# Kernel tuning notes

Hardware: AMD Instinct MI355X
Metric: run time of the kernel (lower is better)

## Reference

```python
import jax, jax.numpy as jnp
import numpy as np

G, NPG, C, H, F, L = 256, 128, 16, 128, 128, 3
N = G * NPG          # 32768 nodes
E = 524288           # 16 edges per node on average
REG, REG_C = 0.01, 0.01
LN_EPS = 1e-5


def setup_inputs() -> dict:
    key = jax.random.key(0)
    ks = jax.random.split(key, 20)
    x = jax.random.normal(ks[0], (N, F), dtype=jnp.float32)
    # edges kept within each graph so dense pooling matches to_dense_batch semantics
    epg = E // G
    offs = jnp.repeat(jnp.arange(G, dtype=jnp.int64) * NPG, epg)
    src = jax.random.randint(ks[1], (E,), 0, NPG, dtype=jnp.int64) + offs
    tgt = jax.random.randint(ks[2], (E,), 0, NPG, dtype=jnp.int64) + offs
    edge_index = jnp.stack([src, tgt])
    mask_breaks = jax.random.bernoulli(ks[3], 0.5, (E,))
    s = jax.random.uniform(ks[4], (N, C), dtype=jnp.float32)
    batch = jnp.repeat(jnp.arange(G, dtype=jnp.int64), NPG)
    sc = 1.0 / np.sqrt(H)
    Wn = jax.random.normal(ks[5], (L, H, H), dtype=jnp.float32) * sc
    bn_ = jax.random.normal(ks[6], (L, H), dtype=jnp.float32) * sc
    Wo = jax.random.normal(ks[7], (L, H, H), dtype=jnp.float32) * sc
    bo = jax.random.normal(ks[8], (L, H), dtype=jnp.float32) * sc
    Wr = jax.random.normal(ks[9], (L, H, H), dtype=jnp.float32) * sc
    ln_g = jnp.ones((L, H), dtype=jnp.float32)
    ln_b = jnp.zeros((L, H), dtype=jnp.float32)
    fln_g = jnp.ones((H,), dtype=jnp.float32)
    fln_b = jnp.zeros((H,), dtype=jnp.float32)
    lin_w = jax.random.normal(ks[10], (1, H), dtype=jnp.float32) * sc
    bias = jnp.zeros((1,), dtype=jnp.float32)
    return {"x": x, "edge_index": edge_index, "mask_breaks": mask_breaks, "s": s,
            "batch": batch, "Wn": Wn, "bn_": bn_, "Wo": Wo, "bo": bo, "Wr": Wr,
            "ln_g": ln_g, "ln_b": ln_b, "fln_g": fln_g, "fln_b": fln_b,
            "lin_w": lin_w, "bias": bias}


def _layernorm(h, g, b):
    mu = jnp.mean(h, axis=-1, keepdims=True)
    v = jnp.mean(jnp.square(h - mu), axis=-1, keepdims=True)
    return (h - mu) * jax.lax.rsqrt(v + LN_EPS) * g + b


def reference(x, edge_index, mask_breaks, s, batch, Wn, bn_, Wo, bo, Wr,
              ln_g, ln_b, fln_g, fln_b, lin_w, bias):
    src, tgt = edge_index[0], edge_index[1]
    ones_e = jnp.ones((E,), dtype=x.dtype)
    cnt = jax.ops.segment_sum(ones_e, tgt, num_segments=N)          # in-degree
    inv_cnt = (1.0 / jnp.maximum(cnt, 1.0))[:, None]
    h = x
    for i in range(L):
        x_in = h @ Wn[i].T + bn_[i]
        x_out = h @ Wo[i].T + bo[i]
        x_root = h @ Wr[i].T
        msg = jnp.where(mask_breaks[:, None], x_in[src], x_out[src])  # [E,H]
        agg = jax.ops.segment_sum(msg, tgt, num_segments=N) * inv_cnt  # mean aggr
        h = jax.nn.relu(_layernorm(agg + x_root, ln_g[i], ln_b[i]))
    # dense per-graph views (equal-size graphs, batch ids sorted -> reshape)
    xd = h.reshape(G, NPG, H)
    sd = s.reshape(G, NPG, C)
    pooled = jnp.einsum("gnc,gnh->gch", sd, xd)                      # [G,C,H]
    pooled = _layernorm(pooled, fln_g, fln_b)
    xc = pooled @ lin_w.T                                            # [G,C,1]
    col_sum = sd.sum(axis=1)                                          # [G,C]
    cmask = (col_sum > 0)[..., None]
    xc = xc * cmask.astype(xc.dtype)
    out = xc.sum(axis=1) + bias                                      # [G,1]
    reg_loss = jnp.abs(Wo).sum() + jnp.abs(bo).sum()
    denom = (cmask.astype(xc.dtype).squeeze(-1) + 1e-7).sum(axis=1, keepdims=True)
    l1_loss = (jnp.abs(xc).sum(axis=1) / denom).mean()
    losses = REG * reg_loss + REG_C * l1_loss
    return out, losses, xc
```

## Files before the change

kernel.cpp:

```cpp
#include <hip/hip_runtime.h>

#define NN   32768
#define HD   128
#define EE   524288
#define GG   256
#define EPG  2048
#define CCd  16
#define LLd  3

typedef short short8 __attribute__((ext_vector_type(8)));
typedef float f32x4 __attribute__((ext_vector_type(4)));

__device__ __forceinline__ unsigned short f2bf(float f) {
  unsigned u = __builtin_bit_cast(unsigned, f);
  return (unsigned short)((u + 0x7FFFu + ((u >> 16) & 1u)) >> 16);
}
__device__ __forceinline__ unsigned bfpack(float a, float b) {
  return (unsigned)f2bf(a) | ((unsigned)f2bf(b) << 16);
}

__global__ __launch_bounds__(256) void convert_w_kernel(const float* __restrict__ Wn, const float* __restrict__ Wo,
                                                        const float* __restrict__ Wr, const float* __restrict__ bo,
                                                        unsigned* __restrict__ Wnb, unsigned* __restrict__ Wob,
                                                        unsigned* __restrict__ Wrb, float* __restrict__ wsreg) {
  int i = blockIdx.x * 256 + threadIdx.x;
  float4 a = *(const float4*)(Wn + (size_t)i * 4);
  float4 b = *(const float4*)(Wo + (size_t)i * 4);
  float4 c = *(const float4*)(Wr + (size_t)i * 4);
  *(uint2*)(Wnb + (size_t)i * 2) = make_uint2(bfpack(a.x, a.y), bfpack(a.z, a.w));
  *(uint2*)(Wob + (size_t)i * 2) = make_uint2(bfpack(b.x, b.y), bfpack(b.z, b.w));
  *(uint2*)(Wrb + (size_t)i * 2) = make_uint2(bfpack(c.x, c.y), bfpack(c.z, c.w));
  float s = fabsf(b.x) + fabsf(b.y) + fabsf(b.z) + fabsf(b.w);
  if (blockIdx.x == 0 && threadIdx.x < 96) {
    float4 d = *(const float4*)(bo + threadIdx.x * 4);
    s += fabsf(d.x) + fabsf(d.y) + fabsf(d.z) + fabsf(d.w);
  }
#pragma unroll
  for (int mk = 1; mk < 64; mk <<= 1) s += __shfl_xor(s, mk, 64);
  if ((threadIdx.x & 63) == 0) atomicAdd(wsreg, s);
}

__global__ __launch_bounds__(256) void build_m_kernel(const int* __restrict__ src, const int* __restrict__ tgt,
                                                      const int* __restrict__ mask,
                                                      unsigned* __restrict__ Mb, float* __restrict__ fin,
                                                      float* __restrict__ fout) {
  __shared__ unsigned Mi[2 * 128 * 64];
  const int g = blockIdx.x;
  const int tid = threadIdx.x;
  for (int i = tid; i < 16384; i += 256) Mi[i] = 0;
  __syncthreads();
  const int e0 = g * EPG;
#pragma unroll
  for (int i = 0; i < 8; ++i) {
    int e = e0 + i * 256 + tid;
    int t = tgt[e] & 127;
    int sl = src[e] & 127;
    int dir = (mask[e] != 0) ? 0 : 1;
    atomicAdd(&Mi[dir * 8192 + t * 64 + (sl >> 1)], 1u << ((sl & 1) * 16));
  }
  __syncthreads();
  const int t = tid >> 1, p = tid & 1;
  unsigned nin = 0, nout = 0;
#pragma unroll 4
  for (int k = 0; k < 32; ++k) { unsigned v = Mi[t * 64 + p * 32 + k]; nin += (v & 0xffffu) + (v >> 16); }
#pragma unroll 4
  for (int k = 0; k < 32; ++k) { unsigned v = Mi[8192 + t * 64 + p * 32 + k]; nout += (v & 0xffffu) + (v >> 16); }
  nin += __shfl_xor((int)nin, 1);
  nout += __shfl_xor((int)nout, 1);
  unsigned dg = nin + nout;
  float inv = 1.0f / (float)(dg > 0 ? dg : 1);
  if (p == 0) { fin[g * 128 + t] = (float)nin * inv; fout[g * 128 + t] = (float)nout * inv; }
#pragma unroll
  for (int dir = 0; dir < 2; ++dir) {
    int base = dir * 8192 + t * 64 + p * 32;
#pragma unroll
    for (int k4 = 0; k4 < 8; ++k4) {
      uint4 v = *(const uint4*)&Mi[base + k4 * 4];
      uint4 o;
      o.x = bfpack((float)(v.x & 0xffffu) * inv, (float)(v.x >> 16) * inv);
      o.y = bfpack((float)(v.y & 0xffffu) * inv, (float)(v.y >> 16) * inv);
      o.z = bfpack((float)(v.z & 0xffffu) * inv, (float)(v.z >> 16) * inv);
      o.w = bfpack((float)(v.w & 0xffffu) * inv, (float)(v.w >> 16) * inv);
      *(uint4*)&Mb[(size_t)g * 16384 + base + k4 * 4] = o;
    }
  }
}

#define SSTR 136
#define YSTR 40
__global__ __launch_bounds__(512) void fused_kernel(
    const float* __restrict__ x, const unsigned short* __restrict__ Mb,
    const unsigned short* __restrict__ Wnb, const unsigned short* __restrict__ Wob,
    const unsigned short* __restrict__ Wrb,
    const float* __restrict__ bn, const float* __restrict__ bo,
    const float* __restrict__ fin, const float* __restrict__ fout,
    const float* __restrict__ lng, const float* __restrict__ lnb,
    const float* __restrict__ s,
    const float* __restrict__ flng, const float* __restrict__ flnb,
    const float* __restrict__ linw, const float* __restrict__ bias,
    float* __restrict__ out, float* __restrict__ l1g) {
  __shared__ unsigned short scratch[128 * SSTR];
  __shared__ unsigned short ys[2 * 128 * YSTR];
  __shared__ unsigned short sTs[16 * SSTR];
  __shared__ float colsumS[CCd];
  __shared__ float xcs[CCd], axcs[CCd], msk[CCd];

  const int g = blockIdx.x;
  const int tid = threadIdx.x;
  const int wave = tid >> 6;
  const int lane = tid & 63;
  const int m = lane & 15;
  const int q = lane >> 4;
  const unsigned short* Mg = Mb + (size_t)g * 32768;
  unsigned* scratch32 = (unsigned*)scratch;

  {
    const float4* xg = (const float4*)(x + (size_t)g * 16384);
#pragma unroll
    for (int i = 0; i < 8; ++i) {
      int flat = i * 512 + tid;
      int t = flat >> 5, f = (flat & 31) << 2;
      float4 v = xg[flat];
      int w0 = (t * SSTR + f) >> 1;
      scratch32[w0] = bfpack(v.x, v.y);
      scratch32[w0 + 1] = bfpack(v.z, v.w);
    }
    int t = tid >> 2, c0 = (tid & 3) << 2;
    float4 v = *(const float4*)(s + (size_t)g * 2048 + t * 16 + c0);
    sTs[(c0 + 0) * SSTR + t] = f2bf(v.x);
    sTs[(c0 + 1) * SSTR + t] = f2bf(v.y);
    sTs[(c0 + 2) * SSTR + t] = f2bf(v.z);
    sTs[(c0 + 3) * SSTR + t] = f2bf(v.w);
    if (tid < CCd) {
      float cs = 0.f;
      for (int tt = 0; tt < 128; ++tt) cs += s[(size_t)g * 2048 + tt * 16 + tid];
      colsumS[tid] = cs;
    }
  }
  __syncthreads();

  for (int L = 0; L < LLd; ++L) {
    const unsigned short* WnL = Wnb + (size_t)L * 16384;
    const unsigned short* WoL = Wob + (size_t)L * 16384;
    const unsigned short* WrL = Wrb + (size_t)L * 16384;
    f32x4 pre[8];
#pragma unroll
    for (int ct = 0; ct < 8; ++ct) pre[ct] = (f32x4){0.f, 0.f, 0.f, 0.f};

#pragma unroll
    for (int ks = 0; ks < 4; ++ks) {
      short8 a = *(const short8*)&scratch[(wave * 16 + m) * SSTR + ks * 32 + q * 8];
#pragma unroll
      for (int ct = 0; ct < 8; ++ct) {
        short8 b = *(const short8*)(WrL + (size_t)(ct * 16 + m) * 128 + ks * 32 + q * 8);
        pre[ct] = __builtin_amdgcn_mfma_f32_16x16x32_bf16(a, b, pre[ct], 0, 0, 0);
      }
    }

    short8 wnf[4], wof[4];
#pragma unroll
    for (int ks = 0; ks < 4; ++ks) {
      wnf[ks] = *(const short8*)(WnL + (size_t)(wave * 16 + m) * 128 + ks * 32 + q * 8);
      wof[ks] = *(const short8*)(WoL + (size_t)(wave * 16 + m) * 128 + ks * 32 + q * 8);
    }

    for (int sc = 0; sc < 4; ++sc) {
      f32x4 ya[2][2];
#pragma unroll
      for (int o2 = 0; o2 < 2; ++o2)
#pragma unroll
        for (int st = 0; st < 2; ++st) ya[o2][st] = (f32x4){0.f, 0.f, 0.f, 0.f};
#pragma unroll
      for (int ks = 0; ks < 4; ++ks) {
        short8 a0 = *(const short8*)&scratch[(sc * 32 + m) * SSTR + ks * 32 + q * 8];
        short8 a1 = *(const short8*)&scratch[(sc * 32 + 16 + m) * SSTR + ks * 32 + q * 8];
        ya[0][0] = __builtin_amdgcn_mfma_f32_16x16x32_bf16(a0, wnf[ks], ya[0][0], 0, 0, 0);
        ya[0][1] = __builtin_amdgcn_mfma_f32_16x16x32_bf16(a1, wnf[ks], ya[0][1], 0, 0, 0);
        ya[1][0] = __builtin_amdgcn_mfma_f32_16x16x32_bf16(a0, wof[ks], ya[1][0], 0, 0, 0);
        ya[1][1] = __builtin_amdgcn_mfma_f32_16x16x32_bf16(a1, wof[ks], ya[1][1], 0, 0, 0);
      }
#pragma unroll
      for (int o2 = 0; o2 < 2; ++o2)
#pragma unroll
        for (int st = 0; st < 2; ++st)
#pragma unroll
          for (int r = 0; r < 4; ++r)
            ys[o2 * 128 * YSTR + (wave * 16 + m) * YSTR + st * 16 + q * 4 + r] = f2bf(ya[o2][st][r]);
      __syncthreads();
#pragma unroll
      for (int o2 = 0; o2 < 2; ++o2) {
        short8 am = *(const short8*)(Mg + (size_t)o2 * 16384 + (size_t)(wave * 16 + m) * 128 + sc * 32 + q * 8);
#pragma unroll
        for (int ct = 0; ct < 8; ++ct) {
          short8 b = *(const short8*)&ys[o2 * 128 * YSTR + (ct * 16 + m) * YSTR + q * 8];
          pre[ct] = __builtin_amdgcn_mfma_f32_16x16x32_bf16(am, b, pre[ct], 0, 0, 0);
        }
      }
      if (sc < 3) __syncthreads();
    }

    float bnv[8], bov[8], gv[8], bv[8];
#pragma unroll
    for (int ct = 0; ct < 8; ++ct) {
      int c = L * 128 + ct * 16 + m;
      bnv[ct] = bn[c]; bov[ct] = bo[c]; gv[ct] = lng[c]; bv[ct] = lnb[c];
    }
#pragma unroll
    for (int r = 0; r < 4; ++r) {
      const int tl = q * 4 + r;
      const int T = g * 128 + wave * 16 + tl;
      const float fiv = fin[T], fov = fout[T];
      float v[8];
      float sum = 0.f;
#pragma unroll
      for (int ct = 0; ct < 8; ++ct) {
        v[ct] = pre[ct][r] + fiv * bnv[ct] + fov * bov[ct];
        sum += v[ct];
      }
      sum += __shfl_xor(sum, 1); sum += __shfl_xor(sum, 2);
      sum += __shfl_xor(sum, 4); sum += __shfl_xor(sum, 8);
      const float mu = sum * (1.0f / 128.0f);
      float sq = 0.f;
#pragma unroll
      for (int ct = 0; ct < 8; ++ct) { float d = v[ct] - mu; sq += d * d; }
      sq += __shfl_xor(sq, 1); sq += __shfl_xor(sq, 2);
      sq += __shfl_xor(sq, 4); sq += __shfl_xor(sq, 8);
      const float rstd = rsqrtf(sq * (1.0f / 128.0f) + 1e-5f);
#pragma unroll
      for (int ct = 0; ct < 8; ++ct) {
        float o = fmaxf((v[ct] - mu) * rstd * gv[ct] + bv[ct], 0.0f);
        scratch[(wave * 16 + tl) * SSTR + ct * 16 + m] = f2bf(o);
      }
    }
    __syncthreads();
  }

  f32x4 pl = (f32x4){0.f, 0.f, 0.f, 0.f};
#pragma unroll
  for (int ks = 0; ks < 4; ++ks) {
    short8 a = *(const short8*)&sTs[m * SSTR + ks * 32 + q * 8];
    short8 b;
#pragma unroll
    for (int j = 0; j < 8; ++j)
      b[j] = (short)scratch[(ks * 32 + q * 8 + j) * SSTR + wave * 16 + m];
    pl = __builtin_amdgcn_mfma_f32_16x16x32_bf16(a, b, pl, 0, 0, 0);
  }
  float* pooledS = (float*)ys;
#pragma unroll
  for (int r = 0; r < 4; ++r) pooledS[(q * 4 + r) * 132 + wave * 16 + m] = pl[r];
  __syncthreads();

  if (tid < 256) {
    const int c = tid >> 4;
    const int j0 = (tid & 15) << 3;
    float v[8];
#pragma unroll
    for (int jj = 0; jj < 8; ++jj) v[jj] = pooledS[c * 132 + j0 + jj];
    float sum = 0.f;
#pragma unroll
    for (int jj = 0; jj < 8; ++jj) sum += v[jj];
#pragma unroll
    for (int mk = 1; mk < 16; mk <<= 1) sum += __shfl_xor(sum, mk, 64);
    float mu = sum * (1.0f / 128.0f);
    float sq = 0.f;
#pragma unroll
    for (int jj = 0; jj < 8; ++jj) { float d = v[jj] - mu; sq += d * d; }
#pragma unroll
    for (int mk = 1; mk < 16; mk <<= 1) sq += __shfl_xor(sq, mk, 64);
    float rstd = rsqrtf(sq * (1.0f / 128.0f) + 1e-5f);
    float dot = 0.f;
#pragma unroll
    for (int jj = 0; jj < 8; ++jj) {
      float nv = (v[jj] - mu) * rstd * flng[j0 + jj] + flnb[j0 + jj];
      dot += nv * linw[j0 + jj];
    }
#pragma unroll
    for (int mk = 1; mk < 16; mk <<= 1) dot += __shfl_xor(dot, mk, 64);
    if ((tid & 15) == 0) {
      float cm = (colsumS[c] > 0.f) ? 1.0f : 0.0f;
      float xcv = dot * cm;
      out[257 + g * CCd + c] = xcv;
      xcs[c] = xcv; axcs[c] = fabsf(xcv); msk[c] = cm;
    }
  }
  __syncthreads();
  if (tid == 0) {
    float so = 0.f, sa = 0.f, sd = 0.f;
#pragma unroll
    for (int k = 0; k < CCd; ++k) { so += xcs[k]; sa += axcs[k]; sd += msk[k] + 1e-7f; }
    out[g] = so + bias[0];
    l1g[g] = sa / sd;
  }
}

__global__ __launch_bounds__(256) void combine_kernel(const float* __restrict__ l1g, const float* __restrict__ wsreg,
                                                      float* __restrict__ outp) {
  const int tid = threadIdx.x;
  float s2 = l1g[tid];
#pragma unroll
  for (int mk = 1; mk < 64; mk <<= 1) s2 += __shfl_xor(s2, mk, 64);
  __shared__ float rs2[4];
  if ((tid & 63) == 0) rs2[tid >> 6] = s2;
  __syncthreads();
  if (tid == 0) {
    float l1 = (rs2[0] + rs2[1] + rs2[2] + rs2[3]) * (1.0f / GG);
    outp[0] = 0.01f * wsreg[0] + 0.01f * l1;
  }
}

extern "C" void kernel_launch(void* const* d_in, const int* in_sizes, int n_in,
                              void* d_out, int out_size, void* d_ws, size_t ws_size,
                              hipStream_t stream) {
  (void)in_sizes; (void)n_in; (void)out_size; (void)ws_size;
  const float* x    = (const float*)d_in[0];
  const int*   ei   = (const int*)d_in[1];
  const int*   mask = (const int*)d_in[2];
  const float* s    = (const float*)d_in[3];
  const float* Wn   = (const float*)d_in[5];
  const float* bn   = (const float*)d_in[6];
  const float* Wo   = (const float*)d_in[7];
  const float* bo   = (const float*)d_in[8];
  const float* Wr   = (const float*)d_in[9];
  const float* lng  = (const float*)d_in[10];
  const float* lnb  = (const float*)d_in[11];
  const float* flng = (const float*)d_in[12];
  const float* flnb = (const float*)d_in[13];
  const float* linw = (const float*)d_in[14];
  const float* bias = (const float*)d_in[15];
  float* out = (float*)d_out;

  char* ws = (char*)d_ws;
  size_t off = 0;
  auto alloc = [&](size_t b) { char* p = ws + off; off += (b + 255) & ~(size_t)255; return p; };
  unsigned short* Mbuf = (unsigned short*)alloc((size_t)GG * 2 * 128 * 128 * 2);
  float* fin    = (float*)alloc((size_t)NN * 4);
  float* fout   = (float*)alloc((size_t)NN * 4);
  unsigned short* Wnb = (unsigned short*)alloc((size_t)LLd * HD * HD * 2);
  unsigned short* Wob = (unsigned short*)alloc((size_t)LLd * HD * HD * 2);
  unsigned short* Wrb = (unsigned short*)alloc((size_t)LLd * HD * HD * 2);
  float* l1g    = (float*)alloc((size_t)GG * 4);
  float* wsreg  = (float*)alloc(256);

  const int* srcA = ei;
  const int* tgtA = ei + EE;

  hipMemsetAsync(wsreg, 0, 4, stream);
  convert_w_kernel<<<LLd * HD * HD / (256 * 4), 256, 0, stream>>>(Wn, Wo, Wr, bo,
      (unsigned*)Wnb, (unsigned*)Wob, (unsigned*)Wrb, wsreg);
  build_m_kernel<<<GG, 256, 0, stream>>>(srcA, tgtA, mask, (unsigned*)Mbuf, fin, fout);
  fused_kernel<<<GG, 512, 0, stream>>>(x, Mbuf, Wnb, Wob, Wrb, bn, bo, fin, fout,
                                       lng, lnb, s, flng, flnb, linw, bias, out, l1g);
  combine_kernel<<<1, 256, 0, stream>>>(l1g, wsreg, out + 256);
}
```

Measured before the change: 163.7 us.

## Merge prep kernels and double-buffer Y tiles in fused GNN layer loop

Merges the weight conversion and adjacency-matrix build into one prep kernel launch, removing a launch. In the fused kernel, the per-chunk Y = h·Wn/Wo products are software-pipelined into a double-buffered LDS tile, so the next chunk's MFMAs overlap the current aggregation and one barrier per step is removed. The adjacency fragments and the fin/fout scalars are hoisted into registers once rather than reloaded every layer. The build-M stores become fully coalesced through a shared inverse-degree table, and the LDS reads are staggered. Costs are more LDS and register pressure, which could lower occupancy.

Measured after the change: 196.2 us. 1.2x slower.

```diff
diff --git a/kernel.cpp b/kernel.cpp
--- a/kernel.cpp
+++ b/kernel.cpp
@@ -7,6 +7,8 @@
 #define EPG  2048
 #define CCd  16
 #define LLd  3
+#define SSTR 136
+#define YSTR 44
 
 typedef short short8 __attribute__((ext_vector_type(8)));
 typedef float f32x4 __attribute__((ext_vector_type(4)));
@@ -18,36 +20,40 @@
 __device__ __forceinline__ unsigned bfpack(float a, float b) {
   return (unsigned)f2bf(a) | ((unsigned)f2bf(b) << 16);
 }
-
-__global__ __launch_bounds__(256) void convert_w_kernel(const float* __restrict__ Wn, const float* __restrict__ Wo,
-                                                        const float* __restrict__ Wr, const float* __restrict__ bo,
-                                                        unsigned* __restrict__ Wnb, unsigned* __restrict__ Wob,
-                                                        unsigned* __restrict__ Wrb, float* __restrict__ wsreg) {
-  int i = blockIdx.x * 256 + threadIdx.x;
-  float4 a = *(const float4*)(Wn + (size_t)i * 4);
-  float4 b = *(const float4*)(Wo + (size_t)i * 4);
-  float4 c = *(const float4*)(Wr + (size_t)i * 4);
-  *(uint2*)(Wnb + (size_t)i * 2) = make_uint2(bfpack(a.x, a.y), bfpack(a.z, a.w));
-  *(uint2*)(Wob + (size_t)i * 2) = make_uint2(bfpack(b.x, b.y), bfpack(b.z, b.w));
-  *(uint2*)(Wrb + (size_t)i * 2) = make_uint2(bfpack(c.x, c.y), bfpack(c.z, c.w));
-  float s = fabsf(b.x) + fabsf(b.y) + fabsf(b.z) + fabsf(b.w);
-  if (blockIdx.x == 0 && threadIdx.x < 96) {
-    float4 d = *(const float4*)(bo + threadIdx.x * 4);
-    s += fabsf(d.x) + fabsf(d.y) + fabsf(d.z) + fabsf(d.w);
-  }
-#pragma unroll
-  for (int mk = 1; mk < 64; mk <<= 1) s += __shfl_xor(s, mk, 64);
-  if ((threadIdx.x & 63) == 0) atomicAdd(wsreg, s);
-}
-
-__global__ __launch_bounds__(256) void build_m_kernel(const int* __restrict__ src, const int* __restrict__ tgt,
-                                                      const int* __restrict__ mask,
-                                                      unsigned* __restrict__ Mb, float* __restrict__ fin,
-                                                      float* __restrict__ fout) {
+#define MFMA __builtin_amdgcn_mfma_f32_16x16x32_bf16
+
+__global__ __launch_bounds__(256) void prep_kernel(const int* __restrict__ src, const int* __restrict__ tgt,
+                                                   const int* __restrict__ mask,
+                                                   const float* __restrict__ Wn, const float* __restrict__ Wo,
+                                                   const float* __restrict__ Wr, const float* __restrict__ bo,
+                                                   unsigned* __restrict__ Mb, float* __restrict__ fin,
+                                                   float* __restrict__ fout,
+                                                   unsigned* __restrict__ Wnb, unsigned* __restrict__ Wob,
+                                                   unsigned* __restrict__ Wrb, float* __restrict__ wsreg) {
   __shared__ unsigned Mi[2 * 128 * 64];
+  __shared__ float invS[128];
+  const int tid = threadIdx.x;
+  if (blockIdx.x >= GG) {
+    int i = (blockIdx.x - GG) * 256 + tid;
+    float4 a = *(const float4*)(Wn + (size_t)i * 4);
+    float4 b = *(const float4*)(Wo + (size_t)i * 4);
+    float4 c = *(const float4*)(Wr + (size_t)i * 4);
+    *(uint2*)(Wnb + (size_t)i * 2) = make_uint2(bfpack(a.x, a.y), bfpack(a.z, a.w));
+    *(uint2*)(Wob + (size_t)i * 2) = make_uint2(bfpack(b.x, b.y), bfpack(b.z, b.w));
+    *(uint2*)(Wrb + (size_t)i * 2) = make_uint2(bfpack(c.x, c.y), bfpack(c.z, c.w));
+    float s = fabsf(b.x) + fabsf(b.y) + fabsf(b.z) + fabsf(b.w);
+    if (blockIdx.x == GG && tid < 96) {
+      float4 d = *(const float4*)(bo + tid * 4);
+      s += fabsf(d.x) + fabsf(d.y) + fabsf(d.z) + fabsf(d.w);
+    }
+#pragma unroll
+    for (int mk = 1; mk < 64; mk <<= 1) s += __shfl_xor(s, mk, 64);
+    if ((tid & 63) == 0) atomicAdd(wsreg, s);
+    return;
+  }
   const int g = blockIdx.x;
-  const int tid = threadIdx.x;
-  for (int i = tid; i < 16384; i += 256) Mi[i] = 0;
+  uint4* Mi4 = (uint4*)Mi;
+  for (int i = tid; i < 4096; i += 256) Mi4[i] = make_uint4(0, 0, 0, 0);
   __syncthreads();
   const int e0 = g * EPG;
 #pragma unroll
@@ -60,34 +66,38 @@
   }
   __syncthreads();
   const int t = tid >> 1, p = tid & 1;
+  const int b0 = t * 64 + p * 32;
   unsigned nin = 0, nout = 0;
-#pragma unroll 4
-  for (int k = 0; k < 32; ++k) { unsigned v = Mi[t * 64 + p * 32 + k]; nin += (v & 0xffffu) + (v >> 16); }
-#pragma unroll 4
-  for (int k = 0; k < 32; ++k) { unsigned v = Mi[8192 + t * 64 + p * 32 + k]; nout += (v & 0xffffu) + (v >> 16); }
+#pragma unroll 8
+  for (int k = 0; k < 32; ++k) { unsigned v = Mi[b0 + ((k + t) & 31)]; nin += (v & 0xffffu) + (v >> 16); }
+#pragma unroll 8
+  for (int k = 0; k < 32; ++k) { unsigned v = Mi[8192 + b0 + ((k + t) & 31)]; nout += (v & 0xffffu) + (v >> 16); }
   nin += __shfl_xor((int)nin, 1);
   nout += __shfl_xor((int)nout, 1);
   unsigned dg = nin + nout;
   float inv = 1.0f / (float)(dg > 0 ? dg : 1);
-  if (p == 0) { fin[g * 128 + t] = (float)nin * inv; fout[g * 128 + t] = (float)nout * inv; }
-#pragma unroll
-  for (int dir = 0; dir < 2; ++dir) {
-    int base = dir * 8192 + t * 64 + p * 32;
-#pragma unroll
-    for (int k4 = 0; k4 < 8; ++k4) {
-      uint4 v = *(const uint4*)&Mi[base + k4 * 4];
-      uint4 o;
-      o.x = bfpack((float)(v.x & 0xffffu) * inv, (float)(v.x >> 16) * inv);
-      o.y = bfpack((float)(v.y & 0xffffu) * inv, (float)(v.y >> 16) * inv);
-      o.z = bfpack((float)(v.z & 0xffffu) * inv, (float)(v.z >> 16) * inv);
-      o.w = bfpack((float)(v.w & 0xffffu) * inv, (float)(v.w >> 16) * inv);
-      *(uint4*)&Mb[(size_t)g * 16384 + base + k4 * 4] = o;
-    }
-  }
-}
-
-#define SSTR 136
-#define YSTR 40
+  if (p == 0) {
+    fin[g * 128 + t] = (float)nin * inv;
+    fout[g * 128 + t] = (float)nout * inv;
+    invS[t] = inv;
+  }
+  __syncthreads();
+  uint4* MbQ = (uint4*)(Mb + (size_t)g * 16384);
+#pragma unroll
+  for (int i = 0; i < 16; ++i) {
+    int f = i * 256 + tid;
+    int tt = (f >> 4) & 127;
+    float iv = invS[tt];
+    uint4 v = Mi4[f];
+    uint4 o;
+    o.x = bfpack((float)(v.x & 0xffffu) * iv, (float)(v.x >> 16) * iv);
+    o.y = bfpack((float)(v.y & 0xffffu) * iv, (float)(v.y >> 16) * iv);
+    o.z = bfpack((float)(v.z & 0xffffu) * iv, (float)(v.z >> 16) * iv);
+    o.w = bfpack((float)(v.w & 0xffffu) * iv, (float)(v.w >> 16) * iv);
+    MbQ[f] = o;
+  }
+}
+
 __global__ __launch_bounds__(512) void fused_kernel(
     const float* __restrict__ x, const unsigned short* __restrict__ Mb,
     const unsigned short* __restrict__ Wnb, const unsigned short* __restrict__ Wob,
@@ -100,7 +110,7 @@
     const float* __restrict__ linw, const float* __restrict__ bias,
     float* __restrict__ out, float* __restrict__ l1g) {
   __shared__ unsigned short scratch[128 * SSTR];
-  __shared__ unsigned short ys[2 * 128 * YSTR];
+  __shared__ unsigned short ys[2][2 * 128 * YSTR];
   __shared__ unsigned short sTs[16 * SSTR];
   __shared__ float colsumS[CCd];
   __shared__ float xcs[CCd], axcs[CCd], msk[CCd];
@@ -137,26 +147,24 @@
       colsumS[tid] = cs;
     }
   }
+  float fivr[4], fovr[4];
+#pragma unroll
+  for (int r = 0; r < 4; ++r) {
+    fivr[r] = fin[g * 128 + wave * 16 + q * 4 + r];
+    fovr[r] = fout[g * 128 + wave * 16 + q * 4 + r];
+  }
+  short8 amf[2][4];
+#pragma unroll
+  for (int o2 = 0; o2 < 2; ++o2)
+#pragma unroll
+    for (int sc = 0; sc < 4; ++sc)
+      amf[o2][sc] = *(const short8*)(Mg + (size_t)o2 * 16384 + (size_t)(wave * 16 + m) * 128 + sc * 32 + q * 8);
   __syncthreads();
 
   for (int L = 0; L < LLd; ++L) {
     const unsigned short* WnL = Wnb + (size_t)L * 16384;
     const unsigned short* WoL = Wob + (size_t)L * 16384;
     const unsigned short* WrL = Wrb + (size_t)L * 16384;
-    f32x4 pre[8];
-#pragma unroll
-    for (int ct = 0; ct < 8; ++ct) pre[ct] = (f32x4){0.f, 0.f, 0.f, 0.f};
-
-#pragma unroll
-    for (int ks = 0; ks < 4; ++ks) {
-      short8 a = *(const short8*)&scratch[(wave * 16 + m) * SSTR + ks * 32 + q * 8];
-#pragma unroll
-      for (int ct = 0; ct < 8; ++ct) {
-        short8 b = *(const short8*)(WrL + (size_t)(ct * 16 + m) * 128 + ks * 32 + q * 8);
-        pre[ct] = __builtin_amdgcn_mfma_f32_16x16x32_bf16(a, b, pre[ct], 0, 0, 0);
-      }
-    }
-
     short8 wnf[4], wof[4];
 #pragma unroll
     for (int ks = 0; ks < 4; ++ks) {
@@ -164,39 +172,82 @@
       wof[ks] = *(const short8*)(WoL + (size_t)(wave * 16 + m) * 128 + ks * 32 + q * 8);
     }
 
+    f32x4 pre[8];
+#pragma unroll
+    for (int ct = 0; ct < 8; ++ct) pre[ct] = (f32x4){0.f, 0.f, 0.f, 0.f};
+
+#pragma unroll
+    for (int ks = 0; ks < 4; ++ks) {
+      short8 a = *(const short8*)&scratch[(wave * 16 + m) * SSTR + ks * 32 + q * 8];
+#pragma unroll
+      for (int ct = 0; ct < 8; ++ct) {
+        short8 b = *(const short8*)(WrL + (size_t)(ct * 16 + m) * 128 + ks * 32 + q * 8);
+        pre[ct] = MFMA(a, b, pre[ct], 0, 0, 0);
+      }
+    }
+
+    {
+      f32x4 ya[2][2];
+#pragma unroll
+      for (int o2 = 0; o2 < 2; ++o2)
+#pragma unroll
+        for (int st = 0; st < 2; ++st) ya[o2][st] = (f32x4){0.f, 0.f, 0.f, 0.f};
+#pragma unroll
+      for (int ks = 0; ks < 4; ++ks) {
+        short8 a0 = *(const short8*)&scratch[(m) * SSTR + ks * 32 + q * 8];
+        short8 a1 = *(const short8*)&scratch[(16 + m) * SSTR + ks * 32 + q * 8];
+        ya[0][0] = MFMA(a0, wnf[ks], ya[0][0], 0, 0, 0);
+        ya[0][1] = MFMA(a1, wnf[ks], ya[0][1], 0, 0, 0);
+        ya[1][0] = MFMA(a0, wof[ks], ya[1][0], 0, 0, 0);
+        ya[1][1] = MFMA(a1, wof[ks], ya[1][1], 0, 0, 0);
+      }
+#pragma unroll
+      for (int o2 = 0; o2 < 2; ++o2)
+#pragma unroll
+        for (int st = 0; st < 2; ++st)
+#pragma unroll
+          for (int r = 0; r < 4; ++r)
+            ys[0][o2 * 128 * YSTR + (wave * 16 + m) * YSTR + st * 16 + q * 4 + r] = f2bf(ya[o2][st][r]);
+    }
+    __syncthreads();
+
+#pragma unroll
     for (int sc = 0; sc < 4; ++sc) {
-      f32x4 ya[2][2];
-#pragma unroll
-      for (int o2 = 0; o2 < 2; ++o2)
-#pragma unroll
-        for (int st = 0; st < 2; ++st) ya[o2][st] = (f32x4){0.f, 0.f, 0.f, 0.f};
-#pragma unroll
-      for (int ks = 0; ks < 4; ++ks) {
-        short8 a0 = *(const short8*)&scratch[(sc * 32 + m) * SSTR + ks * 32 + q * 8];
-        short8 a1 = *(const short8*)&scratch[(sc * 32 + 16 + m) * SSTR + ks * 32 + q * 8];
-        ya[0][0] = __builtin_amdgcn_mfma_f32_16x16x32_bf16(a0, wnf[ks], ya[0][0], 0, 0, 0);
-        ya[0][1] = __builtin_amdgcn_mfma_f32_16x16x32_bf16(a1, wnf[ks], ya[0][1], 0, 0, 0);
-        ya[1][0] = __builtin_amdgcn_mfma_f32_16x16x32_bf16(a0, wof[ks], ya[1][0], 0, 0, 0);
-        ya[1][1] = __builtin_amdgcn_mfma_f32_16x16x32_bf16(a1, wof[ks], ya[1][1], 0, 0, 0);
-      }
-#pragma unroll
-      for (int o2 = 0; o2 < 2; ++o2)
-#pragma unroll
-        for (int st = 0; st < 2; ++st)
-#pragma unroll
-          for (int r = 0; r < 4; ++r)
-            ys[o2 * 128 * YSTR + (wave * 16 + m) * YSTR + st * 16 + q * 4 + r] = f2bf(ya[o2][st][r]);
-      __syncthreads();
-#pragma unroll
-      for (int o2 = 0; o2 < 2; ++o2) {
-        short8 am = *(const short8*)(Mg + (size_t)o2 * 16384 + (size_t)(wave * 16 + m) * 128 + sc * 32 + q * 8);
-#pragma unroll
-        for (int ct = 0; ct < 8; ++ct) {
-          short8 b = *(const short8*)&ys[o2 * 128 * YSTR + (ct * 16 + m) * YSTR + q * 8];
-          pre[ct] = __builtin_amdgcn_mfma_f32_16x16x32_bf16(am, b, pre[ct], 0, 0, 0);
+      f32x4 yb[2][2];
+      if (sc < 3) {
+#pragma unroll
+        for (int o2 = 0; o2 < 2; ++o2)
+#pragma unroll
+          for (int st = 0; st < 2; ++st) yb[o2][st] = (f32x4){0.f, 0.f, 0.f, 0.f};
+#pragma unroll
+        for (int ks = 0; ks < 4; ++ks) {
+          short8 a0 = *(const short8*)&scratch[((sc + 1) * 32 + m) * SSTR + ks * 32 + q * 8];
+          short8 a1 = *(const short8*)&scratch[((sc + 1) * 32 + 16 + m) * SSTR + ks * 32 + q * 8];
+          yb[0][0] = MFMA(a0, wnf[ks], yb[0][0], 0, 0, 0);
+          yb[0][1] = MFMA(a1, wnf[ks], yb[0][1], 0, 0, 0);
+          yb[1][0] = MFMA(a0, wof[ks], yb[1][0], 0, 0, 0);
+          yb[1][1] = MFMA(a1, wof[ks], yb[1][1], 0, 0, 0);
         }
       }
-      if (sc < 3) __syncthreads();
+      const unsigned short* bufc = ys[sc & 1];
+#pragma unroll
+      for (int ct = 0; ct < 8; ++ct) {
+        short8 b0 = *(const short8*)&bufc[(ct * 16 + m) * YSTR + q * 8];
+        short8 b1 = *(const short8*)&bufc[128 * YSTR + (ct * 16 + m) * YSTR + q * 8];
+        pre[ct] = MFMA(amf[0][sc], b0, pre[ct], 0, 0, 0);
+        pre[ct] = MFMA(amf[1][sc], b1, pre[ct], 0, 0, 0);
+      }
+      if (sc < 3) {
+        unsigned short* bufp = ys[(sc + 1) & 1];
+#pragma unroll
+        for (int o2 = 0; o2 < 2; ++o2)
+#pragma unroll
+          for (int st = 0; st < 2; ++st)
+#pragma unroll
+            for (int r = 0; r < 4; ++r)
+              bufp[o2 * 128 * YSTR + (wave * 16 + m) * YSTR + st * 16 + q * 4 + r] = f2bf(yb[o2][st][r]);
+        __syncthreads();
+      }
     }
 
     float bnv[8], bov[8], gv[8], bv[8];
@@ -208,13 +259,11 @@
 #pragma unroll
     for (int r = 0; r < 4; ++r) {
       const int tl = q * 4 + r;
-      const int T = g * 128 + wave * 16 + tl;
-      const float fiv = fin[T], fov = fout[T];
       float v[8];
       float sum = 0.f;
 #pragma unroll
       for (int ct = 0; ct < 8; ++ct) {
-        v[ct] = pre[ct][r] + fiv * bnv[ct] + fov * bov[ct];
+        v[ct] = pre[ct][r] + fivr[r] * bnv[ct] + fovr[r] * bov[ct];
         sum += v[ct];
       }
       sum += __shfl_xor(sum, 1); sum += __shfl_xor(sum, 2);
@@ -235,19 +284,21 @@
     __syncthreads();
   }
 
-  f32x4 pl = (f32x4){0.f, 0.f, 0.f, 0.f};
-#pragma unroll
-  for (int ks = 0; ks < 4; ++ks) {
-    short8 a = *(const short8*)&sTs[m * SSTR + ks * 32 + q * 8];
-    short8 b;
-#pragma unroll
-    for (int j = 0; j < 8; ++j)
-      b[j] = (short)scratch[(ks * 32 + q * 8 + j) * SSTR + wave * 16 + m];
-    pl = __builtin_amdgcn_mfma_f32_16x16x32_bf16(a, b, pl, 0, 0, 0);
-  }
   float* pooledS = (float*)ys;
-#pragma unroll
-  for (int r = 0; r < 4; ++r) pooledS[(q * 4 + r) * 132 + wave * 16 + m] = pl[r];
+  {
+    f32x4 pl = (f32x4){0.f, 0.f, 0.f, 0.f};
+#pragma unroll
+    for (int ks = 0; ks < 4; ++ks) {
+      short8 a = *(const short8*)&sTs[m * SSTR + ks * 32 + q * 8];
+      short8 b;
+#pragma unroll
+      for (int j = 0; j < 8; ++j)
+        b[j] = (short)scratch[(ks * 32 + q * 8 + j) * SSTR + wave * 16 + m];
+      pl = MFMA(a, b, pl, 0, 0, 0);
+    }
+#pragma unroll
+    for (int r = 0; r < 4; ++r) pooledS[(q * 4 + r) * 132 + wave * 16 + m] = pl[r];
+  }
   __syncthreads();
 
   if (tid < 256) {
@@ -345,9 +396,8 @@
   const int* tgtA = ei + EE;
 
   hipMemsetAsync(wsreg, 0, 4, stream);
-  convert_w_kernel<<<LLd * HD * HD / (256 * 4), 256, 0, stream>>>(Wn, Wo, Wr, bo,
-      (unsigned*)Wnb, (unsigned*)Wob, (unsigned*)Wrb, wsreg);
-  build_m_kernel<<<GG, 256, 0, stream>>>(srcA, tgtA, mask, (unsigned*)Mbuf, fin, fout);
+  prep_kernel<<<GG + 48, 256, 0, stream>>>(srcA, tgtA, mask, Wn, Wo, Wr, bo,
+      (unsigned*)Mbuf, fin, fout, (unsigned*)Wnb, (unsigned*)Wob, (unsigned*)Wrb, wsreg);
   fused_kernel<<<GG, 512, 0, stream>>>(x, Mbuf, Wnb, Wob, Wrb, bn, bo, fin, fout,
                                        lng, lnb, s, flng, flnb, linw, bias, out, l1g);
   combine_kernel<<<1, 256, 0, stream>>>(l1g, wsreg, out + 256);
```
